# Performance work log

Measured on AMD Instinct MI355X. Metric: run time of the kernel, lower is better.

## Reference

```python
import jax, jax.numpy as jnp
import numpy as np
from jax import lax

B, IN_C, Q_C, V_C, H, W = 16, 3, 8, 16, 224, 224
K = 7  # static conv kernel size


def _conv(x, w, stride=2, pad=3):
    # x: [N, Cin, H, W], w: [Cout, Cin, kh, kw]
    return lax.conv_general_dilated(
        x, w, (stride, stride), [(pad, pad), (pad, pad)],
        dimension_numbers=("NCHW", "OIHW", "NCHW"))


def _dyn_conv(inp, w):
    # per-sample dynamic conv: inp [C, H, W], w [O, C, kh, kw] -> [O, oh, ow]
    return _conv(inp[None], w, stride=2, pad=3)[0]


def setup_inputs() -> dict:
    key = jax.random.key(0)
    ks = jax.random.split(key, 8)
    x = jax.random.normal(ks[0], (B, IN_C, H, W), dtype=jnp.float32)
    # q_conv_params: input_channel x (weight [q, in, 7, 7], bias [q])
    Wq = jax.random.normal(ks[1], (IN_C, Q_C, IN_C, K, K), dtype=jnp.float32)
    bq = jax.random.normal(ks[2], (IN_C, Q_C), dtype=jnp.float32)
    # k_conv_paramss: input_channel x v_channel x (weight [q, in, 7, 7], bias [q])
    Wk = jax.random.normal(ks[3], (IN_C, V_C, Q_C, IN_C, K, K), dtype=jnp.float32)
    bk = jax.random.normal(ks[4], (IN_C, V_C, Q_C), dtype=jnp.float32)
    # v_conv_param: (weight [v, in, 7, 7], bias [v])
    Wv = jax.random.normal(ks[5], (V_C, IN_C, K, K), dtype=jnp.float32)
    bv = jax.random.normal(ks[6], (V_C,), dtype=jnp.float32)
    return {"x": x, "Wq": Wq, "bq": bq, "Wk": Wk, "bk": bk, "Wv": Wv, "bv": bv}


def reference(x, Wq, bq, Wk, bk, Wv, bv):
    b = x.shape[0]
    in_c, q_c = Wq.shape[0], Wq.shape[1]
    v_c = Wk.shape[1]
    # q: stack of input_channel static convs -> one grouped-by-output conv
    q = _conv(x, Wq.reshape(in_c * q_c, *Wq.shape[2:])) \
        + bq.reshape(-1)[None, :, None, None]
    h2, w2 = q.shape[-2], q.shape[-1]  # 112, 112
    q = q.reshape(b, in_c, q_c, h2, w2)
    # ks: input_channel x v_channel static convs fused into one conv
    kmap = _conv(x, Wk.reshape(in_c * v_c * q_c, *Wk.shape[3:])) \
        + bk.reshape(-1)[None, :, None, None]
    kmap = kmap.reshape(b, in_c, v_c, q_c, h2, w2)
    # a: per (batch, in_c) dynamic conv with feature maps as 112x112 kernels
    # input q[b,i] [q_c, h2, w2], weight kmap[b,i] [v_c, q_c, h2, w2] -> [v_c, 4, 4]
    a = jax.vmap(jax.vmap(_dyn_conv))(q, kmap)  # [B, in_c, v_c, 4, 4]
    # v: static conv
    v = _conv(x, Wv) + bv[None, :, None, None]  # [B, v_c, h2, w2]
    # o: per-batch dynamic conv with a[b] as kernel -> [B, in_c, 58, 58]
    o = jax.vmap(_dyn_conv)(v, a)
    return o
```

## Files before the change

kernel.cpp:

```cpp
#include <hip/hip_runtime.h>
#include <hip/hip_bf16.h>

#define BATCH 16
#define IN_C 3
#define Q_C 8
#define V_C 16
#define HH 224
#define WW 224
#define KK 7

#define XPH 230
#define XPW 232
#define QPH 118
#define QPW 120
#define QP_PLANE (QPH*QPW)
#define QP_QSTRIDE (Q_C*QP_PLANE)

#define PT_MB    202
#define PT2_CHUNKS (BATCH*IN_C*PT_MB*112)
#define PT2_N    ((size_t)PT2_CHUNKS*8)

#define PLANES_N (BATCH*7*IN_C*XPH*QPW)
#define ONES_N   27712
#define VPAD_N   (BATCH*V_C*QPH*QPW)
#define QPADS_N  (BATCH*IN_C*QP_QSTRIDE)
#define D_N      (BATCH*160*384)
#define SPLITS   16
#define DPART_N  (SPLITS*D_N)
#define OUT_N    (BATCH*IN_C*58*58)
#define AW_N     (4*48*192)

typedef __attribute__((ext_vector_type(8))) short bf16x8;
typedef __attribute__((ext_vector_type(4))) float f32x4;
typedef __attribute__((ext_vector_type(4))) unsigned short u16x4;

struct __attribute__((packed, aligned(4))) uint4_a4 { uint4 v; };

static __device__ inline unsigned short f2b(float f) {
    __hip_bfloat16 h = __float2bfloat16(f);
    return *reinterpret_cast<unsigned short*>(&h);
}
static __device__ inline float b2f(unsigned short u) {
    unsigned int v = ((unsigned int)u) << 16;
    return __builtin_bit_cast(float, v);
}
static __device__ inline bf16x8 ld16(const unsigned short* p) {
    return __builtin_bit_cast(bf16x8, *(const uint4*)p);
}

__global__ __launch_bounds__(256) void kX(const float* __restrict__ x,
                                          unsigned short* __restrict__ planes) {
    int idx = blockIdx.x * 256 + threadIdx.x;
    if (idx >= PLANES_N + ONES_N) return;
    if (idx >= PLANES_N) { planes[idx] = 0x3F80; return; }
    int k = idx % QPW;
    int t = idx / QPW;
    int row = t % XPH; t /= XPH;
    int ci = t % IN_C; t /= IN_C;
    int dx = t % 7;
    int b  = t / 7;
    int r = row - 3;
    int c = 2 * k + dx - 3;
    float val = 0.0f;
    if (r >= 0 && r < HH && c >= 0 && c < WW)
        val = x[((size_t)(b * IN_C + ci) * HH + r) * WW + c];
    planes[idx] = f2b(val);
}

__global__ __launch_bounds__(256) void kT(const float* __restrict__ x,
                                          unsigned short* __restrict__ pT2) {
    int chunk = blockIdx.x * 256 + threadIdx.x;
    if (chunk >= PT2_CHUNKS) return;
    int kc = chunk % 112;
    int t2 = chunk / 112;
    int mb = t2 % PT_MB; t2 /= PT_MB;
    int ci = t2 % IN_C;
    int b  = t2 / IN_C;
    const float* xb = x + (size_t)(b * IN_C + ci) * (HH * WW);
    unsigned short pk[8];
    #pragma unroll
    for (int j = 0; j < 8; ++j) {
        int m = 8 * mb + j;
        float val = 0.0f;
        if (m < 1610) {
            int row = m / 7;
            int dx  = m - 7 * row;
            int r = row - 3;
            int c = 2 * kc + dx - 3;
            if (r >= 0 && r < HH && c >= 0 && c < WW)
                val = xb[(size_t)r * WW + c];
        }
        pk[j] = f2b(val);
    }
    *(uint4*)(pT2 + (size_t)chunk * 8) = *(const uint4*)pk;
}

__global__ __launch_bounds__(256) void kW(const float* __restrict__ Wq,
                                          const float* __restrict__ Wv,
                                          unsigned short* __restrict__ Aw2) {
    int idx = blockIdx.x * 256 + threadIdx.x;
    if (idx >= AW_N) return;
    int n = idx % 192;
    int t3 = idx / 192;
    int ch = t3 % 48;
    int p4 = t3 / 48;
    int ci = n / 64;
    int t  = (n % 64) - 2 * p4;
    float v = 0.0f;
    if (ch < 40 && t >= 0 && t < 49) {
        int k = ci * 49 + t;
        v = (ch < 24) ? Wq[(size_t)ch * 147 + k] : Wv[(size_t)(ch - 24) * 147 + k];
    }
    Aw2[idx] = f2b(v);
}

__global__ __launch_bounds__(256) void kA(const unsigned short* __restrict__ pT2,
                                          const unsigned short* __restrict__ Aw2,
                                          const float* __restrict__ bq,
                                          const float* __restrict__ bv,
                                          unsigned short* __restrict__ qpadS,
                                          float* __restrict__ vpad) {
    int g = blockIdx.x;
    int r8 = g & 7, q8 = g >> 3;
    int b  = r8 + 8 * (q8 / 28);
    int yq = q8 % 28;
    int w  = threadIdx.x >> 6;
    int yo = yq * 4 + w;
    int lane = threadIdx.x & 63;
    int cl = lane & 15, kq = lane >> 4;

    int m14 = 14 * yo;
    int p4  = (m14 >> 1) & 3;
    int ms8 = m14 >> 3;

    const unsigned short* AwP = Aw2 + (size_t)p4 * (48 * 192);
    bf16x8 af[3][6];
    #pragma unroll
    for (int mt = 0; mt < 3; ++mt)
        #pragma unroll
        for (int s = 0; s < 6; ++s)
            af[mt][s] = ld16(AwP + (size_t)(mt * 16 + cl) * 192 + s * 32 + kq * 8);

    f32x4 acc[3][7];
    #pragma unroll
    for (int mt = 0; mt < 3; ++mt)
        #pragma unroll
        for (int nt = 0; nt < 7; ++nt)
            acc[mt][nt] = f32x4{0.f, 0.f, 0.f, 0.f};

    #pragma unroll
    for (int s = 0; s < 6; ++s) {
        int ci = s >> 1;
        int mb = ms8 + kq + 4 * (s & 1);
        const unsigned short* bp = pT2
            + ((size_t)((b * IN_C + ci) * PT_MB + mb) * 112) * 8;
        bf16x8 bfr[7];
        #pragma unroll
        for (int nt = 0; nt < 7; ++nt)
            bfr[nt] = ld16(bp + (size_t)(nt * 16 + cl) * 8);
        #pragma unroll
        for (int nt = 0; nt < 7; ++nt)
            #pragma unroll
            for (int mt = 0; mt < 3; ++mt)
                acc[mt][nt] = __builtin_amdgcn_mfma_f32_16x16x32_bf16(af[mt][s], bfr[nt], acc[mt][nt], 0, 0, 0);
    }

    float bias[3][4];
    #pragma unroll
    for (int mt = 0; mt < 3; ++mt)
        #pragma unroll
        for (int r = 0; r < 4; ++r) {
            int ch = mt * 16 + kq * 4 + r;
            bias[mt][r] = (ch < 24) ? bq[ch] : (ch < 40 ? bv[ch - 24] : 0.0f);
        }

    int orow = yo + 3;
    #pragma unroll
    for (int mt = 0; mt < 3; ++mt) {
        #pragma unroll
        for (int nt = 0; nt < 7; ++nt) {
            int kc = nt * 16 + cl;
            #pragma unroll
            for (int r = 0; r < 4; ++r) {
                int ch = mt * 16 + kq * 4 + r;
                float val = acc[mt][nt][r] + bias[mt][r];
                if (ch < 24) {
                    qpadS[((size_t)(b * 3 + (ch >> 3)) * 8 + (ch & 7)) * QP_PLANE
                          + (size_t)orow * QPW + 3 + kc] = f2b(val);
                } else if (ch < 40) {
                    vpad[((size_t)(b * 16 + (ch - 24)) * QPH + orow) * QPW + 3 + kc] = val;
                }
            }
        }
    }
}

__global__ __launch_bounds__(512, 4) void kC(const unsigned short* __restrict__ planes,
                                             const unsigned short* __restrict__ qpadS,
                                             unsigned short* __restrict__ Dpart) {
    int blk = blockIdx.x;
    int b   = blk & 15;
    int nh  = (blk >> 4) & 1;
    int yc  = blk >> 5;
    int tid = threadIdx.x;
    int w = tid >> 6, lane = tid & 63;
    int tt = lane & 15, kq = lane >> 4;
    int th = tt >> 2, tw = tt & 3;

    __shared__ uint4 bs[2][80 * 17];

    int nreal = nh ? 67 : 80;

    if (tid < nreal * 3) {
        int nl = tid / 3, j2 = tid % 3;
        bs[0][nl * 17 + 14 + j2] = uint4{0, 0, 0, 0};
        bs[1][nl * 17 + 14 + j2] = uint4{0, 0, 0, 0};
    } else if (nh == 1) {
        int t2 = tid - nreal * 3;
        if (t2 < 13 * 17) {
            int nl = 67 + t2 / 17, ss = t2 % 17;
            uint4 v = (ss < 14) ? uint4{0x3F803F80u, 0x3F803F80u, 0x3F803F80u, 0x3F803F80u}
                                : uint4{0, 0, 0, 0};
            bs[0][nl * 17 + ss] = v;
            bs[1][nl * 17 + ss] = v;
        }
    }

    int nch = nreal * 14;
    int soff[3];
    int sdst[3];
    bool sact[3];
    #pragma unroll
    for (int i = 0; i < 3; ++i) {
        int c = tid + 512 * i;
        sact[i] = (c < nch);
        int cc2 = sact[i] ? c : 0;
        int nl = cc2 / 14;
        int k0 = (cc2 % 14) * 8;
        int n = nh * 80 + nl;
        int ci = n / 49;
        int rr = n % 49;
        int dy = rr / 7;
        int dx = rr % 7;
        soff[i] = (((b * 7 + dx) * IN_C + ci) * XPH + dy) * QPW + k0;
        sdst[i] = nl * 17 + (k0 >> 3);
    }

    const unsigned short* abase[3];
    #pragma unroll
    for (int j = 0; j < 3; ++j) {
        int tile = w * 3 + j;
        int ic = tile >> 3, qc = tile & 7;
        abase[j] = qpadS + (size_t)(b * IN_C + ic) * QP_QSTRIDE + qc * QP_PLANE
                 + (2 * th) * QPW + 2 * tw;
    }

    f32x4 acc[3][5];
    #pragma unroll
    for (int j = 0; j < 3; ++j)
        #pragma unroll
        for (int nt = 0; nt < 5; ++nt)
            acc[j][nt] = f32x4{0.f, 0.f, 0.f, 0.f};

    int yo0 = yc * 7;
    #pragma unroll
    for (int i = 0; i < 3; ++i)
        if (sact[i]) bs[0][sdst[i]] = *(const uint4*)(planes + soff[i] + yo0 * 240);
    uint4 pf[3];
    #pragma unroll
    for (int i = 0; i < 3; ++i)
        if (sact[i]) pf[i] = *(const uint4*)(planes + soff[i] + (yo0 + 1) * 240);
    __syncthreads();

    for (int ry = 0; ry < 7; ++ry) {
        int yo = yo0 + ry;
        int cur = ry & 1;
        if (ry < 6) {
            #pragma unroll
            for (int i = 0; i < 3; ++i)
                if (sact[i]) bs[cur ^ 1][sdst[i]] = pf[i];
        }
        if (ry < 5) {
            #pragma unroll
            for (int i = 0; i < 3; ++i)
                if (sact[i]) pf[i] = *(const uint4*)(planes + soff[i] + (yo + 2) * 240);
        }
        #pragma unroll
        for (int s = 0; s < 4; ++s) {
            int k = 32 * s + kq * 8;
            int xs = (k < 112) ? k : 96;
            bf16x8 af[3];
            #pragma unroll
            for (int j = 0; j < 3; ++j)
                af[j] = __builtin_bit_cast(bf16x8,
                    ((const uint4_a4*)(abase[j] + yo * QPW + xs))->v);
            #pragma unroll
            for (int nt = 0; nt < 5; ++nt) {
                bf16x8 bf = __builtin_bit_cast(bf16x8, bs[cur][(nt * 16 + tt) * 17 + 4 * s + kq]);
                #pragma unroll
                for (int j = 0; j < 3; ++j)
                    acc[j][nt] = __builtin_amdgcn_mfma_f32_16x16x32_bf16(af[j], bf, acc[j][nt], 0, 0, 0);
            }
        }
        __syncthreads();
    }

    unsigned short* Dp = Dpart + (size_t)(yc * 16 + b) * (160 * 384);
    #pragma unroll
    for (int j = 0; j < 3; ++j) {
        int tile = w * 3 + j;
        int mb = tile * 16 + kq * 4;
        #pragma unroll
        for (int nt = 0; nt < 5; ++nt) {
            int n = nh * 80 + nt * 16 + tt;
            u16x4 pk;
            pk.x = f2b(acc[j][nt][0]);
            pk.y = f2b(acc[j][nt][1]);
            pk.z = f2b(acc[j][nt][2]);
            pk.w = f2b(acc[j][nt][3]);
            *(u16x4*)(Dp + (size_t)n * 384 + mb) = pk;
        }
    }
}

__global__ __launch_bounds__(256) void kR(const unsigned short* __restrict__ Dpart,
                                          float* __restrict__ Df) {
    int idx = blockIdx.x * 256 + threadIdx.x;
    float4 s = float4{0.f, 0.f, 0.f, 0.f};
    #pragma unroll
    for (int yc = 0; yc < SPLITS; ++yc) {
        u16x4 v = *(const u16x4*)(Dpart + (size_t)yc * D_N + 4 * (size_t)idx);
        s.x += b2f(v.x);
        s.y += b2f(v.y);
        s.z += b2f(v.z);
        s.w += b2f(v.w);
    }
    *(float4*)(Df + 4 * (size_t)idx) = s;
}

__global__ __launch_bounds__(256) void kE(const float* __restrict__ Df,
                                          const float* __restrict__ Wk,
                                          const float* __restrict__ bk,
                                          float* __restrict__ a_out) {
    int blk = blockIdx.x;
    int bi = blk >> 4;
    int v  = blk & 15;
    int ic = bi % IN_C;
    int b  = bi / IN_C;
    int tid = threadIdx.x;
    int t  = tid & 15;
    int rl = tid >> 4;
    const float* Dbase = Df + (size_t)b * (160 * 384);
    const float* WkI = Wk + (size_t)(ic * V_C + v) * (Q_C * 147);
    const float* bkI = bk + (ic * V_C + v) * Q_C;
    float s = 0.0f;
    for (int qc = 0; qc < Q_C; ++qc) {
        const float* wrow = WkI + qc * 147;
        int mcol = ic * 128 + qc * 16 + t;
        #pragma unroll
        for (int j = 0; j < 10; ++j) {
            int r = rl + 16 * j;
            if (r < 148) {
                float wv = (r < 147) ? wrow[r] : bkI[qc];
                s = fmaf(wv, Dbase[(size_t)r * 384 + mcol], s);
            }
        }
    }
    __shared__ float red[256];
    red[tid] = s;
    __syncthreads();
    if (tid < 16) {
        float acc2 = 0.f;
        #pragma unroll
        for (int k2 = 0; k2 < 16; ++k2) acc2 += red[k2 * 16 + tid];
        a_out[(size_t)blk * 16 + tid] = acc2;
    }
}

__global__ __launch_bounds__(256) void kO(const float* __restrict__ vpad,
                                          const float* __restrict__ a,
                                          float* __restrict__ out) {
    int idx = blockIdx.x * 256 + threadIdx.x;
    if (idx >= OUT_N) return;
    int ow = idx % 58;
    int t = idx / 58;
    int oh = t % 58; t /= 58;
    int ic = t % IN_C;
    int b  = t / IN_C;
    const float* ab = a + (size_t)(b * IN_C + ic) * (V_C * 16);
    float s = 0.0f;
    for (int vc = 0; vc < V_C; ++vc) {
        const float* vrow = vpad + ((size_t)(b * V_C + vc) * QPH + 2 * oh) * QPW + 2 * ow;
        const float* ar = ab + vc * 16;
        #pragma unroll
        for (int kh = 0; kh < 4; ++kh)
            #pragma unroll
            for (int kw = 0; kw < 4; ++kw)
                s = fmaf(vrow[kh * QPW + kw], ar[kh * 4 + kw], s);
    }
    out[idx] = s;
}

extern "C" void kernel_launch(void* const* d_in, const int* in_sizes, int n_in,
                              void* d_out, int out_size, void* d_ws, size_t ws_size,
                              hipStream_t stream) {
    (void)in_sizes; (void)n_in; (void)out_size; (void)ws_size;
    const float* x  = (const float*)d_in[0];
    const float* Wq = (const float*)d_in[1];
    const float* bq = (const float*)d_in[2];
    const float* Wk = (const float*)d_in[3];
    const float* bk = (const float*)d_in[4];
    const float* Wv = (const float*)d_in[5];
    const float* bv = (const float*)d_in[6];
    float* out = (float*)d_out;

    char* p = (char*)d_ws;
    unsigned short* pT2   = (unsigned short*)p;
    unsigned short* Dpart = (unsigned short*)p;
    p += (size_t)DPART_N * 2;
    unsigned short* planes = (unsigned short*)p;        p += (size_t)(PLANES_N + ONES_N) * 2;
    float*          vpad   = (float*)p;                 p += (size_t)VPAD_N * 4;
    unsigned short* qpadS  = (unsigned short*)p;        p += (size_t)QPADS_N * 2;
    float*          Df     = (float*)p;                 p += (size_t)D_N * 4;
    unsigned short* Aw2    = (unsigned short*)p;        p += (size_t)AW_N * 2;
    float*          a      = (float*)p;

    kX<<<(PLANES_N + ONES_N + 255) / 256, 256, 0, stream>>>(x, planes);
    kT<<<(PT2_CHUNKS + 255) / 256, 256, 0, stream>>>(x, pT2);
    kW<<<(AW_N + 255) / 256, 256, 0, stream>>>(Wq, Wv, Aw2);
    hipMemsetAsync(vpad, 0, (size_t)VPAD_N * 4 + (size_t)QPADS_N * 2, stream);
    kA<<<448, 256, 0, stream>>>(pT2, Aw2, bq, bv, qpadS, vpad);
    kC<<<SPLITS * 2 * 16, 512, 0, stream>>>(planes, qpadS, Dpart);
    kR<<<D_N / 4 / 256, 256, 0, stream>>>(Dpart, Df);
    kE<<<BATCH * IN_C * V_C, 256, 0, stream>>>(Df, Wk, bk, a);
    kO<<<(OUT_N + 255) / 256, 256, 0, stream>>>(vpad, a, out);
}
```

Measured before the change: 198.0 us.

## Fuse input repacking kernels via LDS staging and coalesce kC epilogue stores

Replaces the separate kX and kT repack kernels with one kernel, kXT. It stages an 8-row strip of x in shared memory as bf16 and writes both the strided 'planes' layout and the pT2 layout from it with 16-byte stores. This removes one launch and the duplicated, uncoalesced scalar reads of x. The now-unused trailing ones region of planes is dropped. The kC epilogue now goes through a shared-memory union buffer in two passes, so partial results are written to Dpart as full 16-byte rows rather than scattered 8-byte stores, at the cost of extra barriers.

```diff
diff --git a/kernel.cpp b/kernel.cpp
--- a/kernel.cpp
+++ b/kernel.cpp
@@ -21,7 +21,6 @@
 #define PT2_N    ((size_t)PT2_CHUNKS*8)
 
 #define PLANES_N (BATCH*7*IN_C*XPH*QPW)
-#define ONES_N   27712
 #define VPAD_N   (BATCH*V_C*QPH*QPW)
 #define QPADS_N  (BATCH*IN_C*QP_QSTRIDE)
 #define D_N      (BATCH*160*384)
@@ -48,51 +47,62 @@
     return __builtin_bit_cast(bf16x8, *(const uint4*)p);
 }
 
-__global__ __launch_bounds__(256) void kX(const float* __restrict__ x,
-                                          unsigned short* __restrict__ planes) {
-    int idx = blockIdx.x * 256 + threadIdx.x;
-    if (idx >= PLANES_N + ONES_N) return;
-    if (idx >= PLANES_N) { planes[idx] = 0x3F80; return; }
-    int k = idx % QPW;
-    int t = idx / QPW;
-    int row = t % XPH; t /= XPH;
-    int ci = t % IN_C; t /= IN_C;
-    int dx = t % 7;
-    int b  = t / 7;
-    int r = row - 3;
-    int c = 2 * k + dx - 3;
-    float val = 0.0f;
-    if (r >= 0 && r < HH && c >= 0 && c < WW)
-        val = x[((size_t)(b * IN_C + ci) * HH + r) * WW + c];
-    planes[idx] = f2b(val);
-}
-
-__global__ __launch_bounds__(256) void kT(const float* __restrict__ x,
-                                          unsigned short* __restrict__ pT2) {
-    int chunk = blockIdx.x * 256 + threadIdx.x;
-    if (chunk >= PT2_CHUNKS) return;
-    int kc = chunk % 112;
-    int t2 = chunk / 112;
-    int mb = t2 % PT_MB; t2 /= PT_MB;
-    int ci = t2 % IN_C;
-    int b  = t2 / IN_C;
+__global__ __launch_bounds__(256) void kXT(const float* __restrict__ x,
+                                           unsigned short* __restrict__ planes,
+                                           unsigned short* __restrict__ pT2) {
+    int blk = blockIdx.x;
+    int r0 = blk % 29;
+    int t0 = blk / 29;
+    int ci = t0 % IN_C;
+    int b  = t0 / IN_C;
+    int tid = threadIdx.x;
+
+    __shared__ unsigned short xl[8][240];
+
     const float* xb = x + (size_t)(b * IN_C + ci) * (HH * WW);
-    unsigned short pk[8];
-    #pragma unroll
-    for (int j = 0; j < 8; ++j) {
-        int m = 8 * mb + j;
+    for (int idx = tid; idx < 8 * 240; idx += 256) {
+        int row8 = idx / 240, c = idx % 240;
+        int r = 8 * r0 + row8 - 3;
+        int cc = c - 3;
         float val = 0.0f;
-        if (m < 1610) {
-            int row = m / 7;
-            int dx  = m - 7 * row;
-            int r = row - 3;
-            int c = 2 * kc + dx - 3;
-            if (r >= 0 && r < HH && c >= 0 && c < WW)
-                val = xb[(size_t)r * WW + c];
-        }
-        pk[j] = f2b(val);
-    }
-    *(uint4*)(pT2 + (size_t)chunk * 8) = *(const uint4*)pk;
+        if (r >= 0 && r < HH && cc >= 0 && cc < WW)
+            val = xb[(size_t)r * WW + cc];
+        xl[row8][c] = f2b(val);
+    }
+    __syncthreads();
+
+    for (int t2 = tid; t2 < 784; t2 += 256) {
+        int ko = t2 % 14;
+        int t3 = t2 / 14;
+        int row8 = t3 % 8;
+        int dx = t3 / 8;
+        int prow = 8 * r0 + row8;
+        if (prow >= XPH) continue;
+        unsigned short pk[8];
+        #pragma unroll
+        for (int j = 0; j < 8; ++j)
+            pk[j] = xl[row8][16 * ko + 2 * j + dx];
+        unsigned short* dst = planes
+            + ((size_t)((b * 7 + dx) * IN_C + ci) * XPH + prow) * QPW + 8 * ko;
+        *(uint4*)dst = *(const uint4*)pk;
+    }
+
+    for (int t2 = tid; t2 < 784; t2 += 256) {
+        int kc  = t2 % 112;
+        int mbr = t2 / 112;
+        int mb = 7 * r0 + mbr;
+        if (mb >= PT_MB) continue;
+        unsigned short pk[8];
+        #pragma unroll
+        for (int j = 0; j < 8; ++j) {
+            int mrel = 8 * mbr + j;
+            int row8 = mrel / 7;
+            int dxm  = mrel - 7 * row8;
+            pk[j] = xl[row8][2 * kc + dxm];
+        }
+        unsigned short* dst = pT2 + ((size_t)((b * IN_C + ci) * PT_MB + mb) * 112 + kc) * 8;
+        *(uint4*)dst = *(const uint4*)pk;
+    }
 }
 
 __global__ __launch_bounds__(256) void kW(const float* __restrict__ Wq,
@@ -207,22 +217,25 @@
     int tt = lane & 15, kq = lane >> 4;
     int th = tt >> 2, tw = tt & 3;
 
-    __shared__ uint4 bs[2][80 * 17];
+    __shared__ union {
+        uint4 bs[2][80 * 17];
+        unsigned short dq[40 * 392];
+    } sm;
 
     int nreal = nh ? 67 : 80;
 
     if (tid < nreal * 3) {
         int nl = tid / 3, j2 = tid % 3;
-        bs[0][nl * 17 + 14 + j2] = uint4{0, 0, 0, 0};
-        bs[1][nl * 17 + 14 + j2] = uint4{0, 0, 0, 0};
+        sm.bs[0][nl * 17 + 14 + j2] = uint4{0, 0, 0, 0};
+        sm.bs[1][nl * 17 + 14 + j2] = uint4{0, 0, 0, 0};
     } else if (nh == 1) {
         int t2 = tid - nreal * 3;
         if (t2 < 13 * 17) {
             int nl = 67 + t2 / 17, ss = t2 % 17;
             uint4 v = (ss < 14) ? uint4{0x3F803F80u, 0x3F803F80u, 0x3F803F80u, 0x3F803F80u}
                                 : uint4{0, 0, 0, 0};
-            bs[0][nl * 17 + ss] = v;
-            bs[1][nl * 17 + ss] = v;
+            sm.bs[0][nl * 17 + ss] = v;
+            sm.bs[1][nl * 17 + ss] = v;
         }
     }
 
@@ -265,7 +278,7 @@
     int yo0 = yc * 7;
     #pragma unroll
     for (int i = 0; i < 3; ++i)
-        if (sact[i]) bs[0][sdst[i]] = *(const uint4*)(planes + soff[i] + yo0 * 240);
+        if (sact[i]) sm.bs[0][sdst[i]] = *(const uint4*)(planes + soff[i] + yo0 * 240);
     uint4 pf[3];
     #pragma unroll
     for (int i = 0; i < 3; ++i)
@@ -278,7 +291,7 @@
         if (ry < 6) {
             #pragma unroll
             for (int i = 0; i < 3; ++i)
-                if (sact[i]) bs[cur ^ 1][sdst[i]] = pf[i];
+                if (sact[i]) sm.bs[cur ^ 1][sdst[i]] = pf[i];
         }
         if (ry < 5) {
             #pragma unroll
@@ -296,7 +309,7 @@
                     ((const uint4_a4*)(abase[j] + yo * QPW + xs))->v);
             #pragma unroll
             for (int nt = 0; nt < 5; ++nt) {
-                bf16x8 bf = __builtin_bit_cast(bf16x8, bs[cur][(nt * 16 + tt) * 17 + 4 * s + kq]);
+                bf16x8 bf = __builtin_bit_cast(bf16x8, sm.bs[cur][(nt * 16 + tt) * 17 + 4 * s + kq]);
                 #pragma unroll
                 for (int j = 0; j < 3; ++j)
                     acc[j][nt] = __builtin_amdgcn_mfma_f32_16x16x32_bf16(af[j], bf, acc[j][nt], 0, 0, 0);
@@ -307,18 +320,31 @@
 
     unsigned short* Dp = Dpart + (size_t)(yc * 16 + b) * (160 * 384);
     #pragma unroll
-    for (int j = 0; j < 3; ++j) {
-        int tile = w * 3 + j;
-        int mb = tile * 16 + kq * 4;
-        #pragma unroll
-        for (int nt = 0; nt < 5; ++nt) {
-            int n = nh * 80 + nt * 16 + tt;
-            u16x4 pk;
-            pk.x = f2b(acc[j][nt][0]);
-            pk.y = f2b(acc[j][nt][1]);
-            pk.z = f2b(acc[j][nt][2]);
-            pk.w = f2b(acc[j][nt][3]);
-            *(u16x4*)(Dp + (size_t)n * 384 + mb) = pk;
+    for (int pass = 0; pass < 2; ++pass) {
+        if (pass) __syncthreads();
+        #pragma unroll
+        for (int j = 0; j < 3; ++j) {
+            int tile = w * 3 + j;
+            int mb = tile * 16 + kq * 4;
+            #pragma unroll
+            for (int nt = 0; nt < 5; ++nt) {
+                int nl = nt * 16 + tt;
+                int hi = (nl >= 40) ? 1 : 0;
+                if (hi == pass) {
+                    u16x4 pk;
+                    pk.x = f2b(acc[j][nt][0]);
+                    pk.y = f2b(acc[j][nt][1]);
+                    pk.z = f2b(acc[j][nt][2]);
+                    pk.w = f2b(acc[j][nt][3]);
+                    *(u16x4*)(&sm.dq[(nl - pass * 40) * 392 + mb]) = pk;
+                }
+            }
+        }
+        __syncthreads();
+        for (int c = tid; c < 40 * 48; c += 512) {
+            int nl = c / 48, ms = c % 48;
+            *(uint4*)(Dp + (size_t)(nh * 80 + pass * 40 + nl) * 384 + ms * 8) =
+                *(const uint4*)(&sm.dq[nl * 392 + ms * 8]);
         }
     }
 }
@@ -418,15 +444,14 @@
     unsigned short* pT2   = (unsigned short*)p;
     unsigned short* Dpart = (unsigned short*)p;
     p += (size_t)DPART_N * 2;
-    unsigned short* planes = (unsigned short*)p;        p += (size_t)(PLANES_N + ONES_N) * 2;
+    unsigned short* planes = (unsigned short*)p;        p += (size_t)PLANES_N * 2;
     float*          vpad   = (float*)p;                 p += (size_t)VPAD_N * 4;
     unsigned short* qpadS  = (unsigned short*)p;        p += (size_t)QPADS_N * 2;
     float*          Df     = (float*)p;                 p += (size_t)D_N * 4;
     unsigned short* Aw2    = (unsigned short*)p;        p += (size_t)AW_N * 2;
     float*          a      = (float*)p;
 
-    kX<<<(PLANES_N + ONES_N + 255) / 256, 256, 0, stream>>>(x, planes);
-    kT<<<(PT2_CHUNKS + 255) / 256, 256, 0, stream>>>(x, pT2);
+    kXT<<<BATCH * IN_C * 29, 256, 0, stream>>>(x, planes, pT2);
     kW<<<(AW_N + 255) / 256, 256, 0, stream>>>(Wq, Wv, Aw2);
     hipMemsetAsync(vpad, 0, (size_t)VPAD_N * 4 + (size_t)QPADS_N * 2, stream);
     kA<<<448, 256, 0, stream>>>(pT2, Aw2, bq, bv, qpadS, vpad);
```

New measurement: 188.7 us. -4.7%, faster.
